# Kernel optimization log

Measured on AMD Instinct MI355X. Metric: run time of the kernel, lower is better.

## Reference

```python
import jax, jax.numpy as jnp
import numpy as np

E, H, HD, V, NOUT = 768, 1024, 512, 256, 2  # n_embed, hidden_node, hidden_node_decode, v_attn_dim, n_output


def setup_inputs() -> dict:
    key = jax.random.key(0)
    ks = jax.random.split(key, 16)
    s = 0.02
    B, S = 64, 512
    return {
        "text_fea": jax.random.normal(ks[0], (B, S, E), jnp.float32),
        # gate order along 4H axis: r(input gate), f(forget), g(cell), o(output) -- matches torch module
        "W_in": s * jax.random.normal(ks[1], (E, 4 * H), jnp.float32),
        "b_in": jnp.zeros((4 * H,), jnp.float32),
        "W_h": s * jax.random.normal(ks[2], (H, 4 * H), jnp.float32),
        "b_h": jnp.zeros((4 * H,), jnp.float32),
        "W_ah": s * jax.random.normal(ks[3], (H, V), jnp.float32),
        "b_ah": jnp.zeros((V,), jnp.float32),
        "W_as": s * jax.random.normal(ks[4], (HD, V), jnp.float32),
        "b_as": jnp.zeros((V,), jnp.float32),
        "W_v": s * jax.random.normal(ks[5], (V, 1), jnp.float32),
        "b_v": jnp.zeros((1,), jnp.float32),
        "W_lo": s * jax.random.normal(ks[6], (H, HD), jnp.float32),
        "b_lo": jnp.zeros((HD,), jnp.float32),
        "W_out": s * jax.random.normal(ks[7], (H + HD, NOUT), jnp.float32),
        "b_out": jnp.zeros((NOUT,), jnp.float32),
    }


def _bert_lstm(text_fea, W_in, b_in, W_h, b_h, W_ah, b_ah, W_as, b_as,
               W_v, b_v, W_lo, b_lo, W_out, b_out):
    B, S, _ = text_fea.shape
    # fuse the 4 per-gate input GEMMs for all timesteps into one big GEMM: [B,S,4H]
    xg = jnp.einsum('bse,ef->bsf', text_fea, W_in) + b_in
    xg_t = jnp.transpose(xg, (1, 0, 2))  # [S,B,4H] time-major for scan

    def step(carry, x4):
        h, c = carry
        g4 = x4 + h @ W_h + b_h                      # [B,4H] fused hidden GEMM
        r, f, g, o = jnp.split(g4, 4, axis=-1)
        rt, ft, gt, ot = jax.nn.sigmoid(r), jax.nn.sigmoid(f), jnp.tanh(g), jax.nn.sigmoid(o)
        c = ft * c + rt * gt
        h = ot * jnp.tanh(c)
        return (h, c), h

    h0 = jnp.zeros((B, xg.shape[-1] // 4), text_fea.dtype)
    (h_last, _), hs = jax.lax.scan(step, (h0, h0), xg_t)
    outputs = jnp.transpose(hs, (1, 0, 2))           # [B,S,H]

    final_hidden = h_last @ W_lo + b_lo              # [B,HD]
    WH = jnp.einsum('bsh,hv->bsv', outputs, W_ah) + b_ah
    WS = (final_hidden @ W_as + b_as)[:, None, :]    # broadcast over seq (== repeat in torch)
    score = (jnp.tanh(WH + WS) @ W_v + b_v)[..., 0]  # [B,S]
    attn = jax.nn.softmax(score, axis=-1)
    attention_output = jnp.einsum('bsh,bs->bh', outputs, attn)  # == bmm(outputs^T, attn)
    out = jnp.concatenate([final_hidden, attention_output], axis=1) @ W_out + b_out
    return jax.nn.sigmoid(out)


def reference(text_fea, W_in, b_in, W_h, b_h, W_ah, b_ah, W_as, b_as,
              W_v, b_v, W_lo, b_lo, W_out, b_out):
    return _bert_lstm(text_fea, W_in, b_in, W_h, b_h, W_ah, b_ah, W_as, b_as,
                      W_v, b_v, W_lo, b_lo, W_out, b_out)
```

## Files before the change

### kernel.cpp

```cpp
#include <hip/hip_runtime.h>
#include <hip/hip_bf16.h>
#include <cmath>

typedef __attribute__((ext_vector_type(8))) short short8;
typedef __attribute__((ext_vector_type(4))) short short4_t;
typedef __attribute__((ext_vector_type(4))) float float4_t;

__device__ __forceinline__ float bf2f(unsigned short u) {
    union { unsigned int i; float f; } v; v.i = ((unsigned int)u) << 16; return v.f;
}
__device__ __forceinline__ unsigned short f2bf(float f) {
    union { float f; unsigned int i; } v; v.f = f;
    unsigned int r = v.i + 0x7FFF + ((v.i >> 16) & 1);
    return (unsigned short)(r >> 16);
}
__device__ __forceinline__ float sigm(float x) { return 1.f / (1.f + __expf(-x)); }
__device__ __forceinline__ float tanh_fast(float x) {
    float e = __expf(2.f * x);
    return 1.f - 2.f / (e + 1.f);
}

__device__ __forceinline__ void st_b16_coh(unsigned short* p, unsigned short v) {
    asm volatile("global_store_short %0, %1, off sc0 sc1" :: "v"(p), "v"((unsigned int)v) : "memory");
}
__device__ __forceinline__ float4_t ld_b128_coh_raw(const unsigned short* p) {
    float4_t v;
    asm volatile("global_load_dwordx4 %0, %1, off sc0 sc1" : "=v"(v) : "v"(p));
    return v;
}

__device__ __forceinline__ short8 ld_frag8(const unsigned short* p) {
    short4_t a = *reinterpret_cast<const short4_t*>(p);
    short4_t b = *reinterpret_cast<const short4_t*>(p + 4);
    short8 v;
    v[0]=a[0]; v[1]=a[1]; v[2]=a[2]; v[3]=a[3];
    v[4]=b[0]; v[5]=b[1]; v[6]=b[2]; v[7]=b[3];
    return v;
}


__global__ void k_transpose_bf16(const float* __restrict__ in, unsigned short* __restrict__ out, int R, int C) {
    __shared__ float tile[32][33];
    int c0 = blockIdx.x * 32, r0 = blockIdx.y * 32;
    int tx = threadIdx.x, ty = threadIdx.y;
#pragma unroll
    for (int i = 0; i < 4; i++)
        tile[ty + i * 8][tx] = in[(size_t)(r0 + ty + i * 8) * C + c0 + tx];
    __syncthreads();
#pragma unroll
    for (int i = 0; i < 4; i++)
        out[(size_t)(c0 + ty + i * 8) * R + r0 + tx] = f2bf(tile[tx][ty + i * 8]);
}

__global__ void k_pack_wh(const float* __restrict__ Wh, unsigned short* __restrict__ out) {
    int gid = blockIdx.x * 256 + threadIdx.x;
    int lane = gid & 63, ks = (gid >> 6) & 31, nfrag = gid >> 11;
    int col = (nfrag & 3) * 1024 + ((nfrag >> 2) << 4) + (lane & 15);
    int kb = ks * 32 + ((lane >> 4) << 3);
    short8 v;
#pragma unroll
    for (int e = 0; e < 8; e++) v[e] = (short)f2bf(Wh[(size_t)(kb + e) * 4096 + col]);
    *reinterpret_cast<short8*>(out + (size_t)gid * 8) = v;
}

__global__ void k_pack_win(const float* __restrict__ Win, unsigned short* __restrict__ out) {
    int gid = blockIdx.x * 256 + threadIdx.x;
    int lane = gid & 63;
    int comp = gid >> 6;
    int ks = comp % 24, nfrag = comp / 24;
    int col = (nfrag & 3) * 1024 + ((nfrag >> 2) << 4) + (lane & 15);
    int kb = ks * 32 + ((lane >> 4) << 3);
    short8 v;
#pragma unroll
    for (int e = 0; e < 8; e++) v[e] = (short)f2bf(Win[(size_t)(kb + e) * 4096 + col]);
    *reinterpret_cast<short8*>(out + (size_t)gid * 8) = v;
}

__global__ void k_bias(const float* __restrict__ bi, const float* __restrict__ bh, float* __restrict__ bs) {
    int i = blockIdx.x * 256 + threadIdx.x;
    if (i < 4096) bs[i] = bi[i] + bh[i];
}

__global__ __launch_bounds__(256) void k_gemm_bf16(
    const unsigned short* __restrict__ A,
    const unsigned short* __restrict__ BT,
    unsigned short* __restrict__ C,
    int M, int N, int K)
{
    __shared__ unsigned short Asl[128 * 40];
    __shared__ unsigned short Bsl[128 * 40];
    int t = threadIdx.x, lane = t & 63, w = t >> 6;
    int m0 = blockIdx.y * 128, n0 = blockIdx.x * 128;
    int wm = (w >> 1) * 64, wn = (w & 1) * 64;
    float4_t acc[4][4] = {};

    for (int k0 = 0; k0 < K; k0 += 32) {
        __syncthreads();
#pragma unroll
        for (int p = 0; p < 2; p++) {
            int flat = p * 256 + t;
            int row = flat >> 2, kq = flat & 3;
            short8 va = *reinterpret_cast<const short8*>(A + (size_t)(m0 + row) * K + k0 + kq * 8);
            const short4_t* vp = reinterpret_cast<const short4_t*>(&va);
            *reinterpret_cast<short4_t*>(&Asl[row * 40 + kq * 8]) = vp[0];
            *reinterpret_cast<short4_t*>(&Asl[row * 40 + kq * 8 + 4]) = vp[1];
            short8 vb = *reinterpret_cast<const short8*>(BT + (size_t)(n0 + row) * K + k0 + kq * 8);
            const short4_t* wp = reinterpret_cast<const short4_t*>(&vb);
            *reinterpret_cast<short4_t*>(&Bsl[row * 40 + kq * 8]) = wp[0];
            *reinterpret_cast<short4_t*>(&Bsl[row * 40 + kq * 8 + 4]) = wp[1];
        }
        __syncthreads();
        short8 af[4], bfr[4];
#pragma unroll
        for (int mi = 0; mi < 4; mi++)
            af[mi] = ld_frag8(&Asl[(wm + mi * 16 + (lane & 15)) * 40 + (lane >> 4) * 8]);
#pragma unroll
        for (int ni = 0; ni < 4; ni++)
            bfr[ni] = ld_frag8(&Bsl[(wn + ni * 16 + (lane & 15)) * 40 + (lane >> 4) * 8]);
#pragma unroll
        for (int mi = 0; mi < 4; mi++)
#pragma unroll
            for (int ni = 0; ni < 4; ni++)
                acc[mi][ni] = __builtin_amdgcn_mfma_f32_16x16x32_bf16(af[mi], bfr[ni], acc[mi][ni], 0, 0, 0);
    }

#pragma unroll
    for (int mi = 0; mi < 4; mi++)
#pragma unroll
        for (int ni = 0; ni < 4; ni++)
#pragma unroll
            for (int r = 0; r < 4; r++) {
                int row = m0 + wm + mi * 16 + (lane >> 4) * 4 + r;
                int col = n0 + wn + ni * 16 + (lane & 15);
                C[(size_t)row * N + col] = f2bf(acc[mi][ni][r]);
            }
}

__global__ __launch_bounds__(256, 1) void k_scan(
    const float* __restrict__ text,
    const unsigned short* __restrict__ WhPack,
    const unsigned short* __restrict__ WinPack,
    const float* __restrict__ bias_sum,
    unsigned short* __restrict__ h_bufs,
    unsigned short* __restrict__ hs,
    unsigned int* __restrict__ flags)
{
    __shared__ unsigned short wlds[4 * 32 * 64 * 8];
    __shared__ float part[4 * 4 * 16 * 17];

    int t = threadIdx.x, lane = t & 63, w = t >> 6;
    int bb = blockIdx.x;
    int ut = bb >> 2, mq = bb & 3;
    int u = lane & 15, lq = lane >> 4;
    int ml = t >> 4, u2 = t & 15;
    int brow_c = mq * 16 + ml;
    int jcol = ut * 16 + u2;
    int brow_a = mq * 16 + u;
    float c_reg = 0.f;
    float bsv[4];
#pragma unroll
    for (int g = 0; g < 4; g++) bsv[g] = bias_sum[g * 1024 + jcol];

    const unsigned int* myflag = &flags[((((w << 4) + lane) << 2) + mq) << 4];

    short8 wfx[4][6];
#pragma unroll
    for (int g = 0; g < 4; g++)
#pragma unroll
        for (int kk = 0; kk < 6; kk++)
            wfx[g][kk] = *reinterpret_cast<const short8*>(
                WinPack + (((size_t)((ut * 4 + g) * 24 + w * 6 + kk)) << 9) + lane * 8);

    const unsigned short* wsrc = WhPack + (size_t)ut * 65536;
#pragma unroll
    for (int i = 0; i < 32; i++) {
        int idx = (i * 256 + t) * 8;
        *reinterpret_cast<short8*>(&wlds[idx]) = *reinterpret_cast<const short8*>(wsrc + idx);
    }
    __syncthreads();

    float4_t acc[4];
    {
        const float* tp = text + (size_t)(brow_a * 512 + 0) * 768 + w * 192 + lq * 8;
        float4 f0[6], f1[6];
#pragma unroll
        for (int kk = 0; kk < 6; kk++) {
            f0[kk] = *reinterpret_cast<const float4*>(tp + kk * 32);
            f1[kk] = *reinterpret_cast<const float4*>(tp + kk * 32 + 4);
        }
#pragma unroll
        for (int g = 0; g < 4; g++) acc[g] = (float4_t){0.f, 0.f, 0.f, 0.f};
#pragma unroll
        for (int kk = 0; kk < 6; kk++) {
            short8 a;
            a[0]=(short)f2bf(f0[kk].x); a[1]=(short)f2bf(f0[kk].y);
            a[2]=(short)f2bf(f0[kk].z); a[3]=(short)f2bf(f0[kk].w);
            a[4]=(short)f2bf(f1[kk].x); a[5]=(short)f2bf(f1[kk].y);
            a[6]=(short)f2bf(f1[kk].z); a[7]=(short)f2bf(f1[kk].w);
#pragma unroll
            for (int g = 0; g < 4; g++)
                acc[g] = __builtin_amdgcn_mfma_f32_16x16x32_bf16(a, wfx[g][kk], acc[g], 0, 0, 0);
        }
    }

    for (int ts = 0; ts < 512; ts++) {
        const unsigned short* h_in = h_bufs + (size_t)(ts & 1) * 65536;
        unsigned short* h_out = h_bufs + (size_t)((ts + 1) & 1) * 65536;

        const unsigned short* abase = h_in + (brow_a << 10) + (lq << 3);
        float4_t araw[8];
#pragma unroll
        for (int kk = 0; kk < 8; kk++)
            araw[kk] = ld_b128_coh_raw(abase + (w * 8 + kk) * 32);
        asm volatile("s_waitcnt vmcnt(0)" ::: "memory");
        __builtin_amdgcn_sched_barrier(0);

#pragma unroll
        for (int kk = 0; kk < 8; kk++) {
            short8 a = __builtin_bit_cast(short8, araw[kk]);
#pragma unroll
            for (int g = 0; g < 4; g++) {
                short8 b = *reinterpret_cast<const short8*>(&wlds[((g * 32 + w * 8 + kk) * 64 + lane) * 8]);
                acc[g] = __builtin_amdgcn_mfma_f32_16x16x32_bf16(a, b, acc[g], 0, 0, 0);
            }
        }
#pragma unroll
        for (int g = 0; g < 4; g++)
#pragma unroll
            for (int r = 0; r < 4; r++)
                part[((w * 4 + g) * 16 + lq * 4 + r) * 17 + u] = acc[g][r];
        __syncthreads();

        float gv[4];
#pragma unroll
        for (int g = 0; g < 4; g++) {
            float s = 0.f;
#pragma unroll
            for (int wv = 0; wv < 4; wv++) s += part[((wv * 4 + g) * 16 + ml) * 17 + u2];
            gv[g] = s + bsv[g];
        }
        float rt = sigm(gv[0]), ft = sigm(gv[1]), gt = tanh_fast(gv[2]), ot = sigm(gv[3]);
        c_reg = ft * c_reg + rt * gt;
        float hn = ot * tanh_fast(c_reg);
        unsigned short hb = f2bf(hn);
        st_b16_coh(&h_out[(brow_c << 10) + jcol], hb);

        if (ts != 511) {
            unsigned want = (unsigned)(ts + 1);
            __syncthreads();
            if (t == 0)
                __hip_atomic_store(&flags[bb * 16], want, __ATOMIC_RELAXED, __HIP_MEMORY_SCOPE_AGENT);
            __builtin_nontemporal_store(hb, &hs[(((size_t)(brow_c * 512 + ts)) << 10) + jcol]);

            {
                const float* tp = text + (size_t)(brow_a * 512 + ts + 1) * 768 + w * 192 + lq * 8;
                float4 f0[6], f1[6];
#pragma unroll
                for (int kk = 0; kk < 6; kk++) {
                    f0[kk] = *reinterpret_cast<const float4*>(tp + kk * 32);
                    f1[kk] = *reinterpret_cast<const float4*>(tp + kk * 32 + 4);
                }
#pragma unroll
                for (int g = 0; g < 4; g++) acc[g] = (float4_t){0.f, 0.f, 0.f, 0.f};
#pragma unroll
                for (int kk = 0; kk < 6; kk++) {
                    short8 a;
                    a[0]=(short)f2bf(f0[kk].x); a[1]=(short)f2bf(f0[kk].y);
                    a[2]=(short)f2bf(f0[kk].z); a[3]=(short)f2bf(f0[kk].w);
                    a[4]=(short)f2bf(f1[kk].x); a[5]=(short)f2bf(f1[kk].y);
                    a[6]=(short)f2bf(f1[kk].z); a[7]=(short)f2bf(f1[kk].w);
#pragma unroll
                    for (int g = 0; g < 4; g++)
                        acc[g] = __builtin_amdgcn_mfma_f32_16x16x32_bf16(a, wfx[g][kk], acc[g], 0, 0, 0);
                }
            }

            if (lane < 16) {
                while (__hip_atomic_load(myflag, __ATOMIC_RELAXED, __HIP_MEMORY_SCOPE_AGENT) < want)
                    __builtin_amdgcn_s_sleep(1);
            }
            __builtin_amdgcn_sched_barrier(0);
        } else {
            __builtin_nontemporal_store(hb, &hs[(((size_t)(brow_c * 512 + ts)) << 10) + jcol]);
            __syncthreads();
        }
    }
}


__global__ void k_fh(const unsigned short* __restrict__ h, const float* __restrict__ Wlo,
                     const float* __restrict__ blo, float* __restrict__ fh) {
    int gid = blockIdx.x * 256 + threadIdx.x;
    int b = gid >> 9, d = gid & 511;
    float acc = blo[d];
    for (int k = 0; k < 1024; k++) acc += bf2f(h[b * 1024 + k]) * Wlo[k * 512 + d];
    fh[gid] = acc;
}

__global__ void k_wsb(const float* __restrict__ fh, const float* __restrict__ Was,
                      const float* __restrict__ bas, float* __restrict__ WSb) {
    int gid = blockIdx.x * 256 + threadIdx.x;
    int b = gid >> 8, v = gid & 255;
    float acc = bas[v];
    for (int k = 0; k < 512; k++) acc += fh[b * 512 + k] * Was[k * 256 + v];
    WSb[gid] = acc;
}

__global__ void k_score(const unsigned short* __restrict__ WH, const float* __restrict__ bah,
                        const float* __restrict__ WSb, const float* __restrict__ Wv,
                        const float* __restrict__ bv, float* __restrict__ score) {
    int row = blockIdx.x * 4 + (threadIdx.x >> 6);
    int lane = threadIdx.x & 63;
    int b = row >> 9;
    float acc = 0.f;
#pragma unroll
    for (int q = 0; q < 4; q++) {
        int v = q * 64 + lane;
        float val = bf2f(WH[(size_t)row * 256 + v]) + bah[v] + WSb[b * 256 + v];
        acc += tanhf(val) * Wv[v];
    }
#pragma unroll
    for (int o = 32; o; o >>= 1) acc += __shfl_down(acc, o);
    if (lane == 0) score[row] = acc + bv[0];
}

__global__ __launch_bounds__(512) void k_softmax(const float* __restrict__ score, float* __restrict__ attn) {
    __shared__ float red[8];
    __shared__ float red2[8];
    int b = blockIdx.x, t = threadIdx.x;
    float x = score[b * 512 + t];
    float m = x;
#pragma unroll
    for (int o = 32; o; o >>= 1) m = fmaxf(m, __shfl_xor(m, o));
    if ((t & 63) == 0) red[t >> 6] = m;
    __syncthreads();
    if (t == 0) { float mm = red[0]; for (int i = 1; i < 8; i++) mm = fmaxf(mm, red[i]); red[0] = mm; }
    __syncthreads();
    m = red[0];
    float e = __expf(x - m);
    float s = e;
#pragma unroll
    for (int o = 32; o; o >>= 1) s += __shfl_xor(s, o);
    if ((t & 63) == 0) red2[t >> 6] = s;
    __syncthreads();
    if (t == 0) { float ss = 0.f; for (int i = 0; i < 8; i++) ss += red2[i]; red2[0] = ss; }
    __syncthreads();
    attn[b * 512 + t] = e / red2[0];
}

__global__ void k_attnout(const unsigned short* __restrict__ hs, const float* __restrict__ attn,
                          float* __restrict__ ao) {
    __shared__ float a_s[512];
    int b = blockIdx.x >> 2;
    int hcol = (blockIdx.x & 3) * 256 + threadIdx.x;
    a_s[threadIdx.x] = attn[b * 512 + threadIdx.x];
    a_s[256 + threadIdx.x] = attn[b * 512 + 256 + threadIdx.x];
    __syncthreads();
    float acc = 0.f;
    for (int s = 0; s < 512; s++)
        acc += bf2f(hs[((size_t)(b * 512 + s)) * 1024 + hcol]) * a_s[s];
    ao[b * 1024 + hcol] = acc;
}

__global__ void k_out(const float* __restrict__ fh, const float* __restrict__ ao,
                      const float* __restrict__ Wout, const float* __restrict__ bout,
                      float* __restrict__ out) {
    int t = threadIdx.x;
    if (t >= 128) return;
    int b = t >> 1, o = t & 1;
    float acc = bout[o];
    for (int k = 0; k < 512; k++) acc += fh[b * 512 + k] * Wout[k * 2 + o];
    for (int k = 0; k < 1024; k++) acc += ao[b * 1024 + k] * Wout[(512 + k) * 2 + o];
    out[b * 2 + o] = sigm(acc);
}


extern "C" void kernel_launch(void* const* d_in, const int* in_sizes, int n_in,
                              void* d_out, int out_size, void* d_ws, size_t ws_size,
                              hipStream_t stream) {
    const float* text  = (const float*)d_in[0];
    const float* W_in  = (const float*)d_in[1];
    const float* b_in  = (const float*)d_in[2];
    const float* W_h   = (const float*)d_in[3];
    const float* b_h   = (const float*)d_in[4];
    const float* W_ah  = (const float*)d_in[5];
    const float* b_ah  = (const float*)d_in[6];
    const float* W_as  = (const float*)d_in[7];
    const float* b_as  = (const float*)d_in[8];
    const float* W_v   = (const float*)d_in[9];
    const float* b_v   = (const float*)d_in[10];
    const float* W_lo  = (const float*)d_in[11];
    const float* b_lo  = (const float*)d_in[12];
    const float* W_out = (const float*)d_in[13];
    const float* b_out = (const float*)d_in[14];
    float* out = (float*)d_out;

    char* ws = (char*)d_ws;
    size_t off = 0;
    auto alloc = [&](size_t bytes) {
        void* p = ws + off;
        off = (off + bytes + 255) & ~(size_t)255;
        return p;
    };
    unsigned short* WhPack  = (unsigned short*)alloc((size_t)4096 * 1024 * 2);
    unsigned short* WinPack = (unsigned short*)alloc((size_t)4096 * 768 * 2);
    unsigned short* WahT    = (unsigned short*)alloc((size_t)256 * 1024 * 2);
    float*          biassum = (float*)alloc(4096 * 4);
    unsigned short* hsbuf   = (unsigned short*)alloc((size_t)32768 * 1024 * 2);
    unsigned short* h_bf    = (unsigned short*)alloc((size_t)2 * 65536 * 2);
    unsigned short* WHb     = (unsigned short*)alloc((size_t)32768 * 256 * 2);
    float*          fh      = (float*)alloc(32768 * 4);
    float*          WSb     = (float*)alloc(16384 * 4);
    float*          score   = (float*)alloc(32768 * 4);
    float*          attn    = (float*)alloc(32768 * 4);
    float*          ao      = (float*)alloc(65536 * 4);
    unsigned int*   flags   = (unsigned int*)alloc(256 * 16 * 4);

    dim3 tb(32, 8);
    k_transpose_bf16<<<dim3(256 / 32, 1024 / 32), tb, 0, stream>>>(W_ah, WahT, 1024, 256);
    k_pack_wh<<<2048, 256, 0, stream>>>(W_h, WhPack);
    k_pack_win<<<1536, 256, 0, stream>>>(W_in, WinPack);
    k_bias<<<16, 256, 0, stream>>>(b_in, b_h, biassum);
    hipMemsetAsync(h_bf, 0, (size_t)2 * 65536 * 2, stream);
    hipMemsetAsync(flags, 0, 256 * 16 * 4, stream);

    k_scan<<<256, 256, 0, stream>>>(text, WhPack, WinPack, biassum, h_bf, hsbuf, flags);

    k_fh<<<128, 256, 0, stream>>>(h_bf, W_lo, b_lo, fh);
    k_wsb<<<64, 256, 0, stream>>>(fh, W_as, b_as, WSb);
    k_gemm_bf16<<<dim3(2, 256), 256, 0, stream>>>(hsbuf, WahT, WHb, 32768, 256, 1024);
    k_score<<<8192, 256, 0, stream>>>(WHb, b_ah, WSb, W_v, b_v, score);
    k_softmax<<<64, 512, 0, stream>>>(score, attn);
    k_attnout<<<256, 256, 0, stream>>>(hsbuf, attn, ao);
    k_out<<<1, 128, 0, stream>>>(fh, ao, W_out, b_out, out);
}
```

Measured before the change: 2.311 ms.

## Split scan block into recurrence and input-projection warp groups with LDS ring

Doubles the scan block to 512 threads. Four waves run the hidden-state recurrence, and four new producer waves compute the input projection two timesteps ahead into a small bf16 LDS ring. The goal is to take the input GEMM off the serial critical path between flag waits and overlap it with the recurrent GEMM. In exchange, the x-projection is rounded to bf16 before it is added, and the hs store changes from nontemporal to a normal store. The flag spin is restricted to recurrence waves, while the shared barriers now span all eight waves.

```diff
diff --git a/kernel.cpp b/kernel.cpp
--- a/kernel.cpp
+++ b/kernel.cpp
@@ -136,7 +136,7 @@
             }
 }
 
-__global__ __launch_bounds__(256, 1) void k_scan(
+__global__ __launch_bounds__(512, 1) void k_scan(
     const float* __restrict__ text,
     const unsigned short* __restrict__ WhPack,
     const unsigned short* __restrict__ WinPack,
@@ -147,12 +147,13 @@
 {
     __shared__ unsigned short wlds[4 * 32 * 64 * 8];
     __shared__ float part[4 * 4 * 16 * 17];
+    __shared__ unsigned short ring[4][16][64];
 
     int t = threadIdx.x, lane = t & 63, w = t >> 6;
     int bb = blockIdx.x;
     int ut = bb >> 2, mq = bb & 3;
     int u = lane & 15, lq = lane >> 4;
-    int ml = t >> 4, u2 = t & 15;
+    int ml = (t & 255) >> 4, u2 = t & 15;
     int brow_c = mq * 16 + ml;
     int jcol = ut * 16 + u2;
     int brow_a = mq * 16 + u;
@@ -163,125 +164,123 @@
 
     const unsigned int* myflag = &flags[((((w << 4) + lane) << 2) + mq) << 4];
 
-    short8 wfx[4][6];
-#pragma unroll
-    for (int g = 0; g < 4; g++)
-#pragma unroll
-        for (int kk = 0; kk < 6; kk++)
-            wfx[g][kk] = *reinterpret_cast<const short8*>(
-                WinPack + (((size_t)((ut * 4 + g) * 24 + w * 6 + kk)) << 9) + lane * 8);
+    int gw = w & 3;
+
+    short8 wfx[24];
+    if (w >= 4) {
+#pragma unroll
+        for (int ks = 0; ks < 24; ks++)
+            wfx[ks] = *reinterpret_cast<const short8*>(
+                WinPack + (((size_t)((ut * 4 + gw) * 24 + ks)) << 9) + lane * 8);
+    }
 
     const unsigned short* wsrc = WhPack + (size_t)ut * 65536;
 #pragma unroll
-    for (int i = 0; i < 32; i++) {
-        int idx = (i * 256 + t) * 8;
+    for (int i = 0; i < 16; i++) {
+        int idx = (i * 512 + t) * 8;
         *reinterpret_cast<short8*>(&wlds[idx]) = *reinterpret_cast<const short8*>(wsrc + idx);
     }
-    __syncthreads();
-
-    float4_t acc[4];
-    {
-        const float* tp = text + (size_t)(brow_a * 512 + 0) * 768 + w * 192 + lq * 8;
-        float4 f0[6], f1[6];
-#pragma unroll
-        for (int kk = 0; kk < 6; kk++) {
-            f0[kk] = *reinterpret_cast<const float4*>(tp + kk * 32);
-            f1[kk] = *reinterpret_cast<const float4*>(tp + kk * 32 + 4);
+
+    if (w >= 4) {
+#pragma unroll
+        for (int pt = 0; pt < 2; pt++) {
+            const float* tp = text + ((size_t)(brow_a * 512 + pt)) * 768 + lq * 8;
+            float4_t xacc = {0.f, 0.f, 0.f, 0.f};
+#pragma unroll
+            for (int ks = 0; ks < 24; ks++) {
+                float4 a0 = *reinterpret_cast<const float4*>(tp + ks * 32);
+                float4 a1 = *reinterpret_cast<const float4*>(tp + ks * 32 + 4);
+                short8 a;
+                a[0]=(short)f2bf(a0.x); a[1]=(short)f2bf(a0.y); a[2]=(short)f2bf(a0.z); a[3]=(short)f2bf(a0.w);
+                a[4]=(short)f2bf(a1.x); a[5]=(short)f2bf(a1.y); a[6]=(short)f2bf(a1.z); a[7]=(short)f2bf(a1.w);
+                xacc = __builtin_amdgcn_mfma_f32_16x16x32_bf16(a, wfx[ks], xacc, 0, 0, 0);
+            }
+#pragma unroll
+            for (int r = 0; r < 4; r++)
+                ring[pt][lq * 4 + r][gw * 16 + u] = f2bf(xacc[r]);
         }
-#pragma unroll
-        for (int g = 0; g < 4; g++) acc[g] = (float4_t){0.f, 0.f, 0.f, 0.f};
-#pragma unroll
-        for (int kk = 0; kk < 6; kk++) {
-            short8 a;
-            a[0]=(short)f2bf(f0[kk].x); a[1]=(short)f2bf(f0[kk].y);
-            a[2]=(short)f2bf(f0[kk].z); a[3]=(short)f2bf(f0[kk].w);
-            a[4]=(short)f2bf(f1[kk].x); a[5]=(short)f2bf(f1[kk].y);
-            a[6]=(short)f2bf(f1[kk].z); a[7]=(short)f2bf(f1[kk].w);
-#pragma unroll
-            for (int g = 0; g < 4; g++)
-                acc[g] = __builtin_amdgcn_mfma_f32_16x16x32_bf16(a, wfx[g][kk], acc[g], 0, 0, 0);
-        }
-    }
+    }
+    __syncthreads();
 
     for (int ts = 0; ts < 512; ts++) {
         const unsigned short* h_in = h_bufs + (size_t)(ts & 1) * 65536;
         unsigned short* h_out = h_bufs + (size_t)((ts + 1) & 1) * 65536;
 
-        const unsigned short* abase = h_in + (brow_a << 10) + (lq << 3);
-        float4_t araw[8];
-#pragma unroll
-        for (int kk = 0; kk < 8; kk++)
-            araw[kk] = ld_b128_coh_raw(abase + (w * 8 + kk) * 32);
-        asm volatile("s_waitcnt vmcnt(0)" ::: "memory");
-        __builtin_amdgcn_sched_barrier(0);
-
-#pragma unroll
-        for (int kk = 0; kk < 8; kk++) {
-            short8 a = __builtin_bit_cast(short8, araw[kk]);
+        if (w < 4) {
+            const unsigned short* abase = h_in + (brow_a << 10) + (lq << 3);
+            float4_t araw[8];
+#pragma unroll
+            for (int kk = 0; kk < 8; kk++)
+                araw[kk] = ld_b128_coh_raw(abase + (w * 8 + kk) * 32);
+            asm volatile("s_waitcnt vmcnt(0)" ::: "memory");
+            __builtin_amdgcn_sched_barrier(0);
+
+            float4_t acc[4] = {};
+#pragma unroll
+            for (int kk = 0; kk < 8; kk++) {
+                short8 a = __builtin_bit_cast(short8, araw[kk]);
+#pragma unroll
+                for (int g = 0; g < 4; g++) {
+                    short8 b = *reinterpret_cast<const short8*>(&wlds[((g * 32 + w * 8 + kk) * 64 + lane) * 8]);
+                    acc[g] = __builtin_amdgcn_mfma_f32_16x16x32_bf16(a, b, acc[g], 0, 0, 0);
+                }
+            }
+#pragma unroll
+            for (int g = 0; g < 4; g++)
+#pragma unroll
+                for (int r = 0; r < 4; r++)
+                    part[((w * 4 + g) * 16 + lq * 4 + r) * 17 + u] = acc[g][r];
+        } else {
+            int tt = ts + 2;
+            if (tt < 512) {
+                const float* tp = text + ((size_t)(brow_a * 512 + tt)) * 768 + lq * 8;
+                float4_t xacc = {0.f, 0.f, 0.f, 0.f};
+#pragma unroll
+                for (int ks = 0; ks < 24; ks++) {
+                    float4 a0 = *reinterpret_cast<const float4*>(tp + ks * 32);
+                    float4 a1 = *reinterpret_cast<const float4*>(tp + ks * 32 + 4);
+                    short8 a;
+                    a[0]=(short)f2bf(a0.x); a[1]=(short)f2bf(a0.y); a[2]=(short)f2bf(a0.z); a[3]=(short)f2bf(a0.w);
+                    a[4]=(short)f2bf(a1.x); a[5]=(short)f2bf(a1.y); a[6]=(short)f2bf(a1.z); a[7]=(short)f2bf(a1.w);
+                    xacc = __builtin_amdgcn_mfma_f32_16x16x32_bf16(a, wfx[ks], xacc, 0, 0, 0);
+                }
+                int slot = tt & 3;
+#pragma unroll
+                for (int r = 0; r < 4; r++)
+                    ring[slot][lq * 4 + r][gw * 16 + u] = f2bf(xacc[r]);
+            }
+        }
+        __syncthreads();
+
+        if (w < 4) {
+            float gv[4];
 #pragma unroll
             for (int g = 0; g < 4; g++) {
-                short8 b = *reinterpret_cast<const short8*>(&wlds[((g * 32 + w * 8 + kk) * 64 + lane) * 8]);
-                acc[g] = __builtin_amdgcn_mfma_f32_16x16x32_bf16(a, b, acc[g], 0, 0, 0);
-            }
+                float s = 0.f;
+#pragma unroll
+                for (int wv = 0; wv < 4; wv++) s += part[((wv * 4 + g) * 16 + ml) * 17 + u2];
+                gv[g] = s + bsv[g] + bf2f(ring[ts & 3][ml][g * 16 + u2]);
+            }
+            float rt = sigm(gv[0]), ft = sigm(gv[1]), gt = tanh_fast(gv[2]), ot = sigm(gv[3]);
+            c_reg = ft * c_reg + rt * gt;
+            float hn = ot * tanh_fast(c_reg);
+            unsigned short hb = f2bf(hn);
+            st_b16_coh(&h_out[(brow_c << 10) + jcol], hb);
+            hs[(((size_t)(brow_c * 512 + ts)) << 10) + jcol] = hb;
         }
-#pragma unroll
-        for (int g = 0; g < 4; g++)
-#pragma unroll
-            for (int r = 0; r < 4; r++)
-                part[((w * 4 + g) * 16 + lq * 4 + r) * 17 + u] = acc[g][r];
-        __syncthreads();
-
-        float gv[4];
-#pragma unroll
-        for (int g = 0; g < 4; g++) {
-            float s = 0.f;
-#pragma unroll
-            for (int wv = 0; wv < 4; wv++) s += part[((wv * 4 + g) * 16 + ml) * 17 + u2];
-            gv[g] = s + bsv[g];
-        }
-        float rt = sigm(gv[0]), ft = sigm(gv[1]), gt = tanh_fast(gv[2]), ot = sigm(gv[3]);
-        c_reg = ft * c_reg + rt * gt;
-        float hn = ot * tanh_fast(c_reg);
-        unsigned short hb = f2bf(hn);
-        st_b16_coh(&h_out[(brow_c << 10) + jcol], hb);
 
         if (ts != 511) {
-            unsigned want = (unsigned)(ts + 1);
             __syncthreads();
             if (t == 0)
-                __hip_atomic_store(&flags[bb * 16], want, __ATOMIC_RELAXED, __HIP_MEMORY_SCOPE_AGENT);
-            __builtin_nontemporal_store(hb, &hs[(((size_t)(brow_c * 512 + ts)) << 10) + jcol]);
-
-            {
-                const float* tp = text + (size_t)(brow_a * 512 + ts + 1) * 768 + w * 192 + lq * 8;
-                float4 f0[6], f1[6];
-#pragma unroll
-                for (int kk = 0; kk < 6; kk++) {
-                    f0[kk] = *reinterpret_cast<const float4*>(tp + kk * 32);
-                    f1[kk] = *reinterpret_cast<const float4*>(tp + kk * 32 + 4);
-                }
-#pragma unroll
-                for (int g = 0; g < 4; g++) acc[g] = (float4_t){0.f, 0.f, 0.f, 0.f};
-#pragma unroll
-                for (int kk = 0; kk < 6; kk++) {
-                    short8 a;
-                    a[0]=(short)f2bf(f0[kk].x); a[1]=(short)f2bf(f0[kk].y);
-                    a[2]=(short)f2bf(f0[kk].z); a[3]=(short)f2bf(f0[kk].w);
-                    a[4]=(short)f2bf(f1[kk].x); a[5]=(short)f2bf(f1[kk].y);
-                    a[6]=(short)f2bf(f1[kk].z); a[7]=(short)f2bf(f1[kk].w);
-#pragma unroll
-                    for (int g = 0; g < 4; g++)
-                        acc[g] = __builtin_amdgcn_mfma_f32_16x16x32_bf16(a, wfx[g][kk], acc[g], 0, 0, 0);
-                }
-            }
-
-            if (lane < 16) {
+                __hip_atomic_store(&flags[bb * 16], (unsigned)(ts + 1),
+                                   __ATOMIC_RELAXED, __HIP_MEMORY_SCOPE_AGENT);
+            if (w < 4 && lane < 16) {
+                unsigned want = (unsigned)(ts + 1);
                 while (__hip_atomic_load(myflag, __ATOMIC_RELAXED, __HIP_MEMORY_SCOPE_AGENT) < want)
                     __builtin_amdgcn_s_sleep(1);
             }
             __builtin_amdgcn_sched_barrier(0);
         } else {
-            __builtin_nontemporal_store(hb, &hs[(((size_t)(brow_c * 512 + ts)) << 10) + jcol]);
             __syncthreads();
         }
     }
@@ -424,7 +423,7 @@
     hipMemsetAsync(h_bf, 0, (size_t)2 * 65536 * 2, stream);
     hipMemsetAsync(flags, 0, 256 * 16 * 4, stream);
 
-    k_scan<<<256, 256, 0, stream>>>(text, WhPack, WinPack, biassum, h_bf, hsbuf, flags);
+    k_scan<<<256, 512, 0, stream>>>(text, WhPack, WinPack, biassum, h_bf, hsbuf, flags);
 
     k_fh<<<128, 256, 0, stream>>>(h_bf, W_lo, b_lo, fh);
     k_wsb<<<64, 256, 0, stream>>>(fh, W_as, b_as, WSb);
```

Result: slower. 4.022 ms (+74.0%).
